# Kernel optimization log

Hardware: AMD Instinct MI355X
Metric: run time of the kernel (lower is better)

## Reference

```python
import jax, jax.numpy as jnp
import numpy as np

L, B, T, D, H = 12, 8, 512, 768, 12
DH = D // H
EPS = 1e-12


def _layernorm(x, w, b):
    u = jnp.mean(x, axis=-1, keepdims=True)
    s = jnp.mean(jnp.square(x - u), axis=-1, keepdims=True)
    return w * ((x - u) / jnp.sqrt(s + EPS)) + b


def setup_inputs() -> dict:
    key = jax.random.key(0)
    ks = jax.random.split(key, 8)
    w = lambda k: jax.random.normal(k, (L, D, D), dtype=jnp.float32) * 0.02
    return {
        "query_states": jax.random.normal(ks[0], (B, T, D), dtype=jnp.float32),
        "hidden_states": jax.random.normal(ks[1], (B, T, D), dtype=jnp.float32),
        "attention_mask": jnp.zeros((B, 1, 1, T), dtype=jnp.float32),
        "Wq": w(ks[2]), "bq": jnp.zeros((L, D), jnp.float32),
        "Wk": w(ks[3]), "bk": jnp.zeros((L, D), jnp.float32),
        "Wv": w(ks[4]), "bv": jnp.zeros((L, D), jnp.float32),
        "Wo1": w(ks[5]), "bo1": jnp.zeros((L, D), jnp.float32),
        "ln1_w": jnp.ones((L, D), jnp.float32), "ln1_b": jnp.zeros((L, D), jnp.float32),
        "Wo2": w(ks[6]), "bo2": jnp.zeros((L, D), jnp.float32),
        "ln2_w": jnp.ones((L, D), jnp.float32), "ln2_b": jnp.zeros((L, D), jnp.float32),
    }


def reference(query_states, hidden_states, attention_mask,
              Wq, bq, Wk, bk, Wv, bv,
              Wo1, bo1, ln1_w, ln1_b,
              Wo2, bo2, ln2_w, ln2_b):
    scale = 1.0 / jnp.sqrt(jnp.float32(DH))

    def heads(x):  # [B,T,D] -> [B,H,T,DH]
        return x.reshape(B, T, H, DH).transpose(0, 2, 1, 3)

    def layer_fn(hidden, p):
        (wq, bq_, wk, bk_, wv, bv_, wo1, bo1_, l1w, l1b, wo2, bo2_, l2w, l2b) = p
        q = heads(query_states @ wq + bq_)
        k = heads(hidden @ wk + bk_)
        v = heads(hidden @ wv + bv_)
        scores = jnp.einsum("bhqd,bhkd->bhqk", q, k) * scale + attention_mask
        probs = jax.nn.softmax(scores, axis=-1)
        ctx = jnp.einsum("bhqk,bhkd->bhqd", probs, v)
        ctx = ctx.transpose(0, 2, 1, 3).reshape(B, T, D)
        # attention Output: LN(dense(ctx) + key_states)
        attn_out = _layernorm(ctx @ wo1 + bo1_ + hidden, l1w, l1b)
        # layer Output (intermediate is identity in source): LN(dense(attn_out) + attn_out)
        out = _layernorm(attn_out @ wo2 + bo2_ + attn_out, l2w, l2b)
        return out, None

    params = (Wq, bq, Wk, bk, Wv, bv, Wo1, bo1, ln1_w, ln1_b, Wo2, bo2, ln2_w, ln2_b)
    hidden, _ = jax.lax.scan(layer_fn, hidden_states, params)
    return hidden
```

## Files before the change

### kernel.cpp

```cpp
#include <hip/hip_runtime.h>
#include <stdint.h>

#define L_ 12
#define B_ 8
#define T_ 512
#define D_ 768
#define H_ 12
#define DH_ 64
#define M_ 4096
#define DD_ (D_*D_)

typedef unsigned short u16;
typedef __bf16 bf16x8 __attribute__((ext_vector_type(8)));
typedef float f32x4 __attribute__((ext_vector_type(4)));
typedef u16 u16x4 __attribute__((ext_vector_type(4)));
typedef u16 u16x8 __attribute__((ext_vector_type(8)));

static __device__ __forceinline__ u16 f2b(float f) {
  union { float f; unsigned u; } x; x.f = f;
  unsigned r = x.u + 0x7fffu + ((x.u >> 16) & 1u);
  return (u16)(r >> 16);
}
static __device__ __forceinline__ float b2f(u16 u) {
  union { unsigned u; float f; } x; x.u = ((unsigned)u) << 16; return x.f;
}
static __device__ __forceinline__ void gload16(u16* lds, const u16* g) {
  __builtin_amdgcn_global_load_lds((__attribute__((address_space(1))) void*)(g),
                                   (__attribute__((address_space(3))) void*)(lds), 16, 0, 0);
}
static __device__ __forceinline__ f32x4 mfma16(bf16x8 a, bf16x8 b, f32x4 c) {
  return __builtin_amdgcn_mfma_f32_16x16x32_bf16(a, b, c, 0, 0, 0);
}
static __device__ __forceinline__ bf16x8 ldfrag(const u16* p) {
  return *reinterpret_cast<const bf16x8*>(p);
}

__global__ void init_kernel(const float* __restrict__ qs, const float* __restrict__ hs,
                            u16* __restrict__ qsb, u16* __restrict__ hidb, int n) {
  int i = blockIdx.x * 256 + threadIdx.x;
  if (i < n) {
    qsb[i] = f2b(qs[i]);
    hidb[i] = f2b(hs[i]);
  }
}

__global__ void wt_kernel(const float* W0, const float* W1, const float* W2,
                          const float* W3, const float* W4, u16* __restrict__ out) {
  const int z = blockIdx.z, layer = z / 5, w = z % 5;
  const float* base = (w == 0) ? W0 : (w == 1) ? W1 : (w == 2) ? W2 : (w == 3) ? W3 : W4;
  const float* W = base + (size_t)layer * DD_;
  u16* O = out + (size_t)z * DD_;
  const int nb = blockIdx.x * 64, kb = blockIdx.y * 64;
  __shared__ u16 tile[64][66];
  const int tid = threadIdx.x;
  #pragma unroll
  for (int p = 0; p < 4; ++p) {
    const int idx = p * 256 + tid;
    const int kr = idx >> 4, n4 = (idx & 15) * 4;
    const f32x4 v4 = *reinterpret_cast<const f32x4*>(W + (size_t)(kb + kr) * D_ + nb + n4);
    #pragma unroll
    for (int i = 0; i < 4; i++) tile[n4 + i][kr] = f2b(v4[i]);
  }
  __syncthreads();
  #pragma unroll
  for (int p = 0; p < 4; ++p) {
    const int idx = p * 256 + tid;
    const int n = idx >> 4, k4 = (idx & 15) * 4;
    u16x4 o4;
    #pragma unroll
    for (int i = 0; i < 4; i++) o4[i] = tile[n][k4 + i];
    *reinterpret_cast<u16x4*>(O + (size_t)(nb + n) * D_ + kb + k4) = o4;
  }
}

static __device__ void gemm_core(const u16* __restrict__ A, const u16* __restrict__ W,
                                 const float* __restrict__ bias, const u16* __restrict__ resb,
                                 float* __restrict__ outf, u16* __restrict__ outb,
                                 u16* __restrict__ outv) {
  __shared__ __align__(16) u16 lA[2][64 * 64];
  __shared__ __align__(16) u16 lB[2][128 * 64];
  const int tid = threadIdx.x;
  const int wave = tid >> 6, lane = tid & 63;
  const int wm = wave >> 1, wn = wave & 1;

  const int nbx = gridDim.x;
  const int nwg = nbx * gridDim.y;
  const int orig = blockIdx.y * nbx + blockIdx.x;
  const int cpx = nwg >> 3;
  const int swz = (orig & 7) * cpx + (orig >> 3);
  const int m0 = (swz / nbx) * 64, n0 = (swz % nbx) * 128;
  const int lr = lane & 15, lg = lane >> 4;

  f32x4 acc[2][4];
  #pragma unroll
  for (int i = 0; i < 2; i++)
    #pragma unroll
    for (int j = 0; j < 4; j++) acc[i][j] = f32x4{0.f, 0.f, 0.f, 0.f};

  const int uA0 = wave * 64 + lane, uA1 = 256 + uA0;
  const int rA0 = uA0 >> 3, cA0 = ((uA0 & 7) ^ (rA0 & 7)) << 3;
  const int rA1 = uA1 >> 3, cA1 = ((uA1 & 7) ^ (rA1 & 7)) << 3;
  const u16* Ab0 = A + (size_t)(m0 + rA0) * D_ + cA0;
  const u16* Ab1 = A + (size_t)(m0 + rA1) * D_ + cA1;
  const u16* Wb[4];
  #pragma unroll
  for (int q = 0; q < 4; ++q) {
    const int u = q * 256 + wave * 64 + lane;
    const int r = u >> 3, c = ((u & 7) ^ (r & 7)) << 3;
    Wb[q] = W + (size_t)(n0 + r) * D_ + c;
  }

#define STAGE(buf, k0_) do {                                   \
    gload16(lA[buf] + wave * 512,        Ab0 + (k0_));         \
    gload16(lA[buf] + 2048 + wave * 512, Ab1 + (k0_));         \
    gload16(lB[buf] + wave * 512,        Wb[0] + (k0_));       \
    gload16(lB[buf] + 2048 + wave * 512, Wb[1] + (k0_));       \
    gload16(lB[buf] + 4096 + wave * 512, Wb[2] + (k0_));       \
    gload16(lB[buf] + 6144 + wave * 512, Wb[3] + (k0_));       \
  } while (0)

  STAGE(0, 0);
  __syncthreads();

  const int sx = lr & 7;

  int cur = 0;
  for (int kt = 0; kt < 12; ++kt) {
    if (kt < 11) STAGE(cur ^ 1, (kt + 1) * 64);
    bf16x8 af[2][2], bw[2][4];
    #pragma unroll
    for (int kk = 0; kk < 2; ++kk) {
      const int uo = ((kk * 4 + lg) ^ sx) << 3;
      #pragma unroll
      for (int i = 0; i < 2; i++)
        af[kk][i] = ldfrag(lA[cur] + ((wm * 32 + i * 16 + lr) << 6) + uo);
      #pragma unroll
      for (int j = 0; j < 4; j++)
        bw[kk][j] = ldfrag(lB[cur] + ((wn * 64 + j * 16 + lr) << 6) + uo);
    }
    #pragma unroll
    for (int kk = 0; kk < 2; ++kk)
      #pragma unroll
      for (int i = 0; i < 2; i++)
        #pragma unroll
        for (int j = 0; j < 4; j++)
          acc[i][j] = mfma16(af[kk][i], bw[kk][j], acc[i][j]);
    __syncthreads();
    cur ^= 1;
  }
#undef STAGE

  if (outv) {
    #pragma unroll
    for (int j = 0; j < 4; j++) {
      const int colg = n0 + wn * 64 + j * 16 + lr;
      const float bv = bias[colg];
      const int h = colg >> 6, dh = colg & 63;
      #pragma unroll
      for (int i = 0; i < 2; i++) {
        const int rowb = m0 + wm * 32 + i * 16 + lg * 4;
        const int bb = rowb >> 9, t = rowb & 511;
        u16x4 o4;
        #pragma unroll
        for (int r = 0; r < 4; r++) o4[r] = f2b(acc[i][j][r] + bv);
        *reinterpret_cast<u16x4*>(outv + ((size_t)((bb * H_ + h) * DH_ + dh)) * T_ + t) = o4;
      }
    }
    return;
  }
  #pragma unroll
  for (int j = 0; j < 4; j++) {
    const int colg = n0 + wn * 64 + j * 16 + lr;
    const float bv = bias[colg];
    #pragma unroll
    for (int i = 0; i < 2; i++) {
      const int rowb = m0 + wm * 32 + i * 16 + lg * 4;
      #pragma unroll
      for (int r = 0; r < 4; r++) {
        float v = acc[i][j][r] + bv;
        const size_t off = (size_t)(rowb + r) * D_ + colg;
        if (resb) v += b2f(resb[off]);
        if (outf) outf[off] = v;
        if (outb) outb[off] = f2b(v);
      }
    }
  }
}

__global__ __launch_bounds__(256) void qall_kernel(const u16* qsb, const u16* wt60,
                                                   const float* bq, u16* qall) {
  const int l = blockIdx.z;
  gemm_core(qsb, wt60 + (size_t)l * 5 * DD_, bq + l * D_, nullptr,
            nullptr, qall + (size_t)l * M_ * D_, nullptr);
}

__global__ __launch_bounds__(256) void kv_kernel(const u16* hidb,
                                                 const u16* wk, const u16* wv,
                                                 const float* bk, const float* bv,
                                                 u16* kout, u16* vtout) {
  if (blockIdx.z == 0) gemm_core(hidb, wk, bk, nullptr, nullptr, kout, nullptr);
  else                 gemm_core(hidb, wv, bv, nullptr, nullptr, nullptr, vtout);
}

__global__ __launch_bounds__(256) void qkv3_kernel(const u16* qsb, const u16* hidb,
                                                   const u16* wq, const u16* wk, const u16* wv,
                                                   const float* bq, const float* bk, const float* bv,
                                                   u16* q, u16* kout, u16* vtout) {
  if (blockIdx.z == 0)      gemm_core(qsb,  wq, bq, nullptr, nullptr, q, nullptr);
  else if (blockIdx.z == 1) gemm_core(hidb, wk, bk, nullptr, nullptr, kout, nullptr);
  else                      gemm_core(hidb, wv, bv, nullptr, nullptr, nullptr, vtout);
}

__global__ __launch_bounds__(256) void o_kernel(const u16* A, const u16* W, const float* bias,
                                                const u16* resb, float* outf) {
  gemm_core(A, W, bias, resb, outf, nullptr, nullptr);
}

__global__ __launch_bounds__(256) void attn_kernel(const u16* __restrict__ q, const u16* __restrict__ k,
                                                   const u16* __restrict__ vt, const float* __restrict__ mask,
                                                   u16* __restrict__ ctx) {
  __shared__ __align__(16) u16 KT[2][64 * 64];
  __shared__ __align__(16) u16 VT[2][64 * 64];
  __shared__ __align__(16) u16 PT[4 * 16 * 64];
  const int tid = threadIdx.x, wave = tid >> 6, lane = tid & 63;
  const int id = blockIdx.x;
  const int bh = id % 96, qblk = id / 96;
  const int b = bh / H_, h = bh % H_;
  const int q0 = qblk * 64 + wave * 16;
  const int lr = lane & 15, lg = lane >> 4;

  bf16x8 qa0, qa1;
  {
    const u16* qp = q + (size_t)(b * T_ + q0 + lr) * D_ + h * DH_ + lg * 8;
    qa0 = ldfrag(qp);
    qa1 = ldfrag(qp + 32);
  }

  const int su0 = wave * 64 + lane, su1 = 256 + wave * 64 + lane;
  const int sr0 = su0 >> 3, sc0 = ((su0 & 7) ^ (sr0 & 7)) << 3;
  const int sr1 = su1 >> 3, sc1 = ((su1 & 7) ^ (sr1 & 7)) << 3;
  const u16* kbase = k + (size_t)b * T_ * D_ + h * DH_;
  const u16* vbase = vt + (size_t)bh * DH_ * T_;

#define STAGEKV(buf, kt_) do {                                                         \
    gload16(KT[buf] + wave * 512,        kbase + (size_t)((kt_) * 64 + sr0) * D_ + sc0); \
    gload16(KT[buf] + 2048 + wave * 512, kbase + (size_t)((kt_) * 64 + sr1) * D_ + sc1); \
    gload16(VT[buf] + wave * 512,        vbase + (size_t)sr0 * T_ + (kt_) * 64 + sc0);   \
    gload16(VT[buf] + 2048 + wave * 512, vbase + (size_t)sr1 * T_ + (kt_) * 64 + sc1);   \
  } while (0)

  float mrow[4] = {-1e30f, -1e30f, -1e30f, -1e30f};
  float lrow[4] = {0.f, 0.f, 0.f, 0.f};
  f32x4 O[4] = { {0,0,0,0}, {0,0,0,0}, {0,0,0,0}, {0,0,0,0} };
  u16* Pw = PT + wave * 1024;

  STAGEKV(0, 0);
  int cur = 0;
  for (int kt = 0; kt < 8; ++kt) {
    __syncthreads();
    if (kt < 7) STAGEKV(cur ^ 1, kt + 1);

    f32x4 S[4];
    #pragma unroll
    for (int nf = 0; nf < 4; ++nf) {
      const u16* kr = KT[cur] + (nf * 16 + lr) * 64;
      bf16x8 kb0 = ldfrag(kr + ((lg       ^ (lr & 7)) << 3));
      bf16x8 kb1 = ldfrag(kr + (((4 + lg) ^ (lr & 7)) << 3));
      f32x4 a = {0.f, 0.f, 0.f, 0.f};
      a = mfma16(qa0, kb0, a);
      a = mfma16(qa1, kb1, a);
      S[nf] = a;
    }
    #pragma unroll
    for (int nf = 0; nf < 4; ++nf) {
      const float mk = mask[(size_t)b * T_ + kt * 64 + nf * 16 + lr];
      #pragma unroll
      for (int r = 0; r < 4; r++) S[nf][r] = S[nf][r] * 0.125f + mk;
    }
    #pragma unroll
    for (int r = 0; r < 4; r++) {
      float tm = fmaxf(fmaxf(S[0][r], S[1][r]), fmaxf(S[2][r], S[3][r]));
      #pragma unroll
      for (int d = 1; d <= 8; d <<= 1) tm = fmaxf(tm, __shfl_xor(tm, d));
      const float mn = fmaxf(mrow[r], tm);
      const float sc = __expf(mrow[r] - mn);
      float ts = 0.f;
      #pragma unroll
      for (int nf = 0; nf < 4; ++nf) { float pv = __expf(S[nf][r] - mn); S[nf][r] = pv; ts += pv; }
      #pragma unroll
      for (int d = 1; d <= 8; d <<= 1) ts += __shfl_xor(ts, d);
      lrow[r] = lrow[r] * sc + ts;
      mrow[r] = mn;
      #pragma unroll
      for (int nf = 0; nf < 4; ++nf) O[nf][r] *= sc;
    }
    #pragma unroll
    for (int nf = 0; nf < 4; ++nf)
      #pragma unroll
      for (int r = 0; r < 4; r++) {
        const int R = lg * 4 + r;
        Pw[R * 64 + ((((nf << 1) | (lr >> 3)) ^ (R & 7)) << 3) + (lr & 7)] = f2b(S[nf][r]);
      }
    #pragma unroll
    for (int ks = 0; ks < 2; ++ks) {
      bf16x8 pa = ldfrag(Pw + lr * 64 + (((ks * 4 + lg) ^ (lr & 7)) << 3));
      #pragma unroll
      for (int nf = 0; nf < 4; ++nf) {
        bf16x8 vb = ldfrag(VT[cur] + (nf * 16 + lr) * 64 + (((ks * 4 + lg) ^ (lr & 7)) << 3));
        O[nf] = mfma16(pa, vb, O[nf]);
      }
    }
    cur ^= 1;
  }
#undef STAGEKV

  #pragma unroll
  for (int r = 0; r < 4; r++) {
    const float inv = 1.f / lrow[r];
    const int row = q0 + lg * 4 + r;
    #pragma unroll
    for (int nf = 0; nf < 4; ++nf)
      ctx[(size_t)(b * T_ + row) * D_ + h * DH_ + nf * 16 + lr] = f2b(O[nf][r] * inv);
  }
}

__global__ __launch_bounds__(256) void ln_kernel(const float* __restrict__ y,
                                                 const float* __restrict__ w, const float* __restrict__ bp,
                                                 float* __restrict__ outf, u16* __restrict__ outb) {
  const int wave = threadIdx.x >> 6, lane = threadIdx.x & 63;
  const int row = blockIdx.x * 4 + wave;
  const f32x4* yp = (const f32x4*)(y + (size_t)row * D_);
  f32x4 x[3];
  #pragma unroll
  for (int j = 0; j < 3; j++) x[j] = yp[j * 64 + lane];
  float s = 0.f;
  #pragma unroll
  for (int j = 0; j < 3; j++) s += x[j][0] + x[j][1] + x[j][2] + x[j][3];
  #pragma unroll
  for (int d = 1; d <= 32; d <<= 1) s += __shfl_xor(s, d);
  const float u = s * (1.f / D_);
  float v = 0.f;
  #pragma unroll
  for (int j = 0; j < 3; j++)
    #pragma unroll
    for (int c = 0; c < 4; c++) { float t = x[j][c] - u; v += t * t; }
  #pragma unroll
  for (int d = 1; d <= 32; d <<= 1) v += __shfl_xor(v, d);
  const float rinv = rsqrtf(v * (1.f / D_) + 1e-12f);
  const f32x4* wp = (const f32x4*)w;
  const f32x4* bpp = (const f32x4*)bp;
  #pragma unroll
  for (int j = 0; j < 3; j++) {
    const f32x4 w4 = wp[j * 64 + lane];
    const f32x4 b4 = bpp[j * 64 + lane];
    f32x4 o4;
    u16x4 ob;
    #pragma unroll
    for (int c = 0; c < 4; c++) {
      o4[c] = w4[c] * ((x[j][c] - u) * rinv) + b4[c];
      ob[c] = f2b(o4[c]);
    }
    if (outf) ((f32x4*)(outf + (size_t)row * D_))[j * 64 + lane] = o4;
    ((u16x4*)(outb + (size_t)row * D_))[j * 64 + lane] = ob;
  }
}

extern "C" void kernel_launch(void* const* d_in, const int* in_sizes, int n_in,
                              void* d_out, int out_size, void* d_ws, size_t ws_size,
                              hipStream_t stream) {
  const float* qs   = (const float*)d_in[0];
  const float* hs   = (const float*)d_in[1];
  const float* mask = (const float*)d_in[2];
  const float* Wq   = (const float*)d_in[3];
  const float* bq   = (const float*)d_in[4];
  const float* Wk   = (const float*)d_in[5];
  const float* bk   = (const float*)d_in[6];
  const float* Wv   = (const float*)d_in[7];
  const float* bv   = (const float*)d_in[8];
  const float* Wo1  = (const float*)d_in[9];
  const float* bo1  = (const float*)d_in[10];
  const float* l1w  = (const float*)d_in[11];
  const float* l1b  = (const float*)d_in[12];
  const float* Wo2  = (const float*)d_in[13];
  const float* bo2  = (const float*)d_in[14];
  const float* l2w  = (const float*)d_in[15];
  const float* l2b  = (const float*)d_in[16];
  float* out = (float*)d_out;

  char* p = (char*)d_ws;
  auto alloc = [&](size_t bytes) { char* r = p; p += (bytes + 255) & ~(size_t)255; return r; };
  u16*   qsb  = (u16*)alloc((size_t)M_ * D_ * 2);
  u16*   hidb = (u16*)alloc((size_t)M_ * D_ * 2);
  u16*   kb_  = (u16*)alloc((size_t)M_ * D_ * 2);
  u16*   vtb  = (u16*)alloc((size_t)M_ * D_ * 2);
  u16*   ctxb = (u16*)alloc((size_t)M_ * D_ * 2);
  float* y    = (float*)alloc((size_t)M_ * D_ * 4);
  u16*   aob  = (u16*)alloc((size_t)M_ * D_ * 2);
  u16*   qb   = (u16*)alloc((size_t)M_ * D_ * 2);
  const size_t base_used = (size_t)(p - (char*)d_ws);
  const size_t wt60_bytes = (size_t)60 * DD_ * 2;
  const size_t qall_bytes = (size_t)12 * M_ * D_ * 2;
  const bool wt_once  = (ws_size - base_used) >= wt60_bytes + 512;
  u16* wt60 = (u16*)alloc(wt_once ? wt60_bytes : (size_t)5 * DD_ * 2);
  const size_t used2 = (size_t)(p - (char*)d_ws);
  const bool q_all   = wt_once && (ws_size - used2) >= qall_bytes + 512;
  u16* qall = q_all ? (u16*)alloc(qall_bytes) : qb;

  init_kernel<<<(M_ * D_ + 255) / 256, 256, 0, stream>>>(qs, hs, qsb, hidb, M_ * D_);
  if (wt_once)
    wt_kernel<<<dim3(12, 12, 60), 256, 0, stream>>>(Wq, Wk, Wv, Wo1, Wo2, wt60);
  if (q_all)
    qall_kernel<<<dim3(6, 64, 12), 256, 0, stream>>>(qsb, wt60, bq, qall);

  for (int l = 0; l < L_; ++l) {
    const size_t wo = (size_t)l * DD_;
    u16* wt = wt_once ? (wt60 + (size_t)l * 5 * DD_) : wt60;
    if (!wt_once)
      wt_kernel<<<dim3(12, 12, 5), 256, 0, stream>>>(Wq + wo, Wk + wo, Wv + wo, Wo1 + wo, Wo2 + wo, wt);
    const u16* qcur;
    if (q_all) {
      qcur = qall + (size_t)l * M_ * D_;
      kv_kernel<<<dim3(6, 64, 2), 256, 0, stream>>>(hidb, wt + DD_, wt + 2 * DD_,
                                                    bk + l * D_, bv + l * D_, kb_, vtb);
    } else {
      qcur = qb;
      qkv3_kernel<<<dim3(6, 64, 3), 256, 0, stream>>>(qsb, hidb,
          wt, wt + DD_, wt + 2 * DD_, bq + l * D_, bk + l * D_, bv + l * D_, qb, kb_, vtb);
    }
    attn_kernel<<<768, 256, 0, stream>>>(qcur, kb_, vtb, mask, ctxb);
    o_kernel<<<dim3(6, 64), 256, 0, stream>>>(ctxb, wt + 3 * DD_, bo1 + l * D_, hidb, y);
    ln_kernel<<<1024, 256, 0, stream>>>(y, l1w + l * D_, l1b + l * D_, nullptr, aob);
    o_kernel<<<dim3(6, 64), 256, 0, stream>>>(aob, wt + 4 * DD_, bo2 + l * D_, aob, y);
    ln_kernel<<<1024, 256, 0, stream>>>(y, l2w + l * D_, l2b + l * D_,
                                        (l == L_ - 1) ? out : nullptr, hidb);
  }
}
```

Measured before the change: 1.326 ms.

## Add 128x128 GEMM for hoisted Q projection, bf16 pre-LN buffer, attention setprio

Adds a 128x128-tile GEMM core with workgroup swizzling and uses it for the hoisted all-layer Q projection, halving that grid. Stores the pre-layernorm sums in bf16 rather than fp32, which halves the y traffic but adds rounding before LayerNorm. Raises wave priority around the MFMA blocks in attention and pairs rows in the weight transpose so LDS stores are 32-bit. These are several loosely related tweaks, and the bf16 intermediate reduces accuracy.

Result: faster. 1.115 ms, median of 2 (-15.9%).

```diff
diff --git a/kernel.cpp b/kernel.cpp
--- a/kernel.cpp
+++ b/kernel.cpp
@@ -13,8 +13,8 @@
 typedef unsigned short u16;
 typedef __bf16 bf16x8 __attribute__((ext_vector_type(8)));
 typedef float f32x4 __attribute__((ext_vector_type(4)));
+typedef u16 u16x2 __attribute__((ext_vector_type(2)));
 typedef u16 u16x4 __attribute__((ext_vector_type(4)));
-typedef u16 u16x8 __attribute__((ext_vector_type(8)));
 
 static __device__ __forceinline__ u16 f2b(float f) {
   union { float f; unsigned u; } x; x.f = f;
@@ -54,12 +54,16 @@
   __shared__ u16 tile[64][66];
   const int tid = threadIdx.x;
   #pragma unroll
-  for (int p = 0; p < 4; ++p) {
+  for (int p = 0; p < 2; ++p) {
     const int idx = p * 256 + tid;
-    const int kr = idx >> 4, n4 = (idx & 15) * 4;
-    const f32x4 v4 = *reinterpret_cast<const f32x4*>(W + (size_t)(kb + kr) * D_ + nb + n4);
-    #pragma unroll
-    for (int i = 0; i < 4; i++) tile[n4 + i][kr] = f2b(v4[i]);
+    const int rp = idx >> 4, n4 = (idx & 15) * 4;
+    const f32x4 a = *reinterpret_cast<const f32x4*>(W + (size_t)(kb + 2 * rp) * D_ + nb + n4);
+    const f32x4 b = *reinterpret_cast<const f32x4*>(W + (size_t)(kb + 2 * rp + 1) * D_ + nb + n4);
+    #pragma unroll
+    for (int i = 0; i < 4; i++) {
+      u16x2 pr; pr[0] = f2b(a[i]); pr[1] = f2b(b[i]);
+      *reinterpret_cast<u16x2*>(&tile[n4 + i][2 * rp]) = pr;
+    }
   }
   __syncthreads();
   #pragma unroll
@@ -187,11 +191,96 @@
   }
 }
 
+static __device__ void gemm128_core(const u16* __restrict__ A, const u16* __restrict__ W,
+                                    const float* __restrict__ bias, u16* __restrict__ outb) {
+  __shared__ __align__(16) u16 lA[2][128 * 64];
+  __shared__ __align__(16) u16 lB[2][128 * 64];
+  const int tid = threadIdx.x;
+  const int wave = tid >> 6, lane = tid & 63;
+  const int wm = wave >> 1, wn = wave & 1;
+
+  const int nbx = gridDim.x;
+  const int nwg = nbx * gridDim.y;
+  const int orig = blockIdx.y * nbx + blockIdx.x;
+  const int cpx = nwg >> 3;
+  const int swz = (orig & 7) * cpx + (orig >> 3);
+  const int m0 = (swz / nbx) * 128, n0 = (swz % nbx) * 128;
+  const int lr = lane & 15, lg = lane >> 4;
+
+  f32x4 acc[4][4];
+  #pragma unroll
+  for (int i = 0; i < 4; i++)
+    #pragma unroll
+    for (int j = 0; j < 4; j++) acc[i][j] = f32x4{0.f, 0.f, 0.f, 0.f};
+
+  const u16* Ab[4];
+  const u16* Wb[4];
+  #pragma unroll
+  for (int q = 0; q < 4; ++q) {
+    const int u = q * 256 + wave * 64 + lane;
+    const int r = u >> 3, c = ((u & 7) ^ (r & 7)) << 3;
+    Ab[q] = A + (size_t)(m0 + r) * D_ + c;
+    Wb[q] = W + (size_t)(n0 + r) * D_ + c;
+  }
+
+#define STAGE128(buf, k0_) do {                                \
+    gload16(lA[buf] + wave * 512,        Ab[0] + (k0_));       \
+    gload16(lA[buf] + 2048 + wave * 512, Ab[1] + (k0_));       \
+    gload16(lA[buf] + 4096 + wave * 512, Ab[2] + (k0_));       \
+    gload16(lA[buf] + 6144 + wave * 512, Ab[3] + (k0_));       \
+    gload16(lB[buf] + wave * 512,        Wb[0] + (k0_));       \
+    gload16(lB[buf] + 2048 + wave * 512, Wb[1] + (k0_));       \
+    gload16(lB[buf] + 4096 + wave * 512, Wb[2] + (k0_));       \
+    gload16(lB[buf] + 6144 + wave * 512, Wb[3] + (k0_));       \
+  } while (0)
+
+  STAGE128(0, 0);
+  __syncthreads();
+
+  const int sx = lr & 7;
+
+  int cur = 0;
+  for (int kt = 0; kt < 12; ++kt) {
+    if (kt < 11) STAGE128(cur ^ 1, (kt + 1) * 64);
+    #pragma unroll
+    for (int kk = 0; kk < 2; ++kk) {
+      const int uo = ((kk * 4 + lg) ^ sx) << 3;
+      bf16x8 af[4], bw[4];
+      #pragma unroll
+      for (int i = 0; i < 4; i++)
+        af[i] = ldfrag(lA[cur] + ((wm * 64 + i * 16 + lr) << 6) + uo);
+      #pragma unroll
+      for (int j = 0; j < 4; j++)
+        bw[j] = ldfrag(lB[cur] + ((wn * 64 + j * 16 + lr) << 6) + uo);
+      #pragma unroll
+      for (int i = 0; i < 4; i++)
+        #pragma unroll
+        for (int j = 0; j < 4; j++)
+          acc[i][j] = mfma16(af[i], bw[j], acc[i][j]);
+    }
+    __syncthreads();
+    cur ^= 1;
+  }
+#undef STAGE128
+
+  #pragma unroll
+  for (int j = 0; j < 4; j++) {
+    const int colg = n0 + wn * 64 + j * 16 + lr;
+    const float bv = bias[colg];
+    #pragma unroll
+    for (int i = 0; i < 4; i++) {
+      const int rowb = m0 + wm * 64 + i * 16 + lg * 4;
+      #pragma unroll
+      for (int r = 0; r < 4; r++)
+        outb[(size_t)(rowb + r) * D_ + colg] = f2b(acc[i][j][r] + bv);
+    }
+  }
+}
+
 __global__ __launch_bounds__(256) void qall_kernel(const u16* qsb, const u16* wt60,
                                                    const float* bq, u16* qall) {
   const int l = blockIdx.z;
-  gemm_core(qsb, wt60 + (size_t)l * 5 * DD_, bq + l * D_, nullptr,
-            nullptr, qall + (size_t)l * M_ * D_, nullptr);
+  gemm128_core(qsb, wt60 + (size_t)l * 5 * DD_, bq + l * D_, qall + (size_t)l * M_ * D_);
 }
 
 __global__ __launch_bounds__(256) void kv_kernel(const u16* hidb,
@@ -212,8 +301,8 @@
 }
 
 __global__ __launch_bounds__(256) void o_kernel(const u16* A, const u16* W, const float* bias,
-                                                const u16* resb, float* outf) {
-  gemm_core(A, W, bias, resb, outf, nullptr, nullptr);
+                                                const u16* resb, u16* yb) {
+  gemm_core(A, W, bias, resb, nullptr, yb, nullptr);
 }
 
 __global__ __launch_bounds__(256) void attn_kernel(const u16* __restrict__ q, const u16* __restrict__ k,
@@ -261,6 +350,7 @@
     if (kt < 7) STAGEKV(cur ^ 1, kt + 1);
 
     f32x4 S[4];
+    __builtin_amdgcn_s_setprio(1);
     #pragma unroll
     for (int nf = 0; nf < 4; ++nf) {
       const u16* kr = KT[cur] + (nf * 16 + lr) * 64;
@@ -271,6 +361,7 @@
       a = mfma16(qa1, kb1, a);
       S[nf] = a;
     }
+    __builtin_amdgcn_s_setprio(0);
     #pragma unroll
     for (int nf = 0; nf < 4; ++nf) {
       const float mk = mask[(size_t)b * T_ + kt * 64 + nf * 16 + lr];
@@ -301,6 +392,7 @@
         const int R = lg * 4 + r;
         Pw[R * 64 + ((((nf << 1) | (lr >> 3)) ^ (R & 7)) << 3) + (lr & 7)] = f2b(S[nf][r]);
       }
+    __builtin_amdgcn_s_setprio(1);
     #pragma unroll
     for (int ks = 0; ks < 2; ++ks) {
       bf16x8 pa = ldfrag(Pw + lr * 64 + (((ks * 4 + lg) ^ (lr & 7)) << 3));
@@ -310,6 +402,7 @@
         O[nf] = mfma16(pa, vb, O[nf]);
       }
     }
+    __builtin_amdgcn_s_setprio(0);
     cur ^= 1;
   }
 #undef STAGEKV
@@ -324,15 +417,19 @@
   }
 }
 
-__global__ __launch_bounds__(256) void ln_kernel(const float* __restrict__ y,
+__global__ __launch_bounds__(256) void ln_kernel(const u16* __restrict__ y,
                                                  const float* __restrict__ w, const float* __restrict__ bp,
                                                  float* __restrict__ outf, u16* __restrict__ outb) {
   const int wave = threadIdx.x >> 6, lane = threadIdx.x & 63;
   const int row = blockIdx.x * 4 + wave;
-  const f32x4* yp = (const f32x4*)(y + (size_t)row * D_);
+  const u16x4* yp = (const u16x4*)(y + (size_t)row * D_);
   f32x4 x[3];
   #pragma unroll
-  for (int j = 0; j < 3; j++) x[j] = yp[j * 64 + lane];
+  for (int j = 0; j < 3; j++) {
+    const u16x4 r4 = yp[j * 64 + lane];
+    #pragma unroll
+    for (int c = 0; c < 4; c++) x[j][c] = b2f(r4[c]);
+  }
   float s = 0.f;
   #pragma unroll
   for (int j = 0; j < 3; j++) s += x[j][0] + x[j][1] + x[j][2] + x[j][3];
@@ -394,7 +491,7 @@
   u16*   kb_  = (u16*)alloc((size_t)M_ * D_ * 2);
   u16*   vtb  = (u16*)alloc((size_t)M_ * D_ * 2);
   u16*   ctxb = (u16*)alloc((size_t)M_ * D_ * 2);
-  float* y    = (float*)alloc((size_t)M_ * D_ * 4);
+  u16*   yb   = (u16*)alloc((size_t)M_ * D_ * 2);
   u16*   aob  = (u16*)alloc((size_t)M_ * D_ * 2);
   u16*   qb   = (u16*)alloc((size_t)M_ * D_ * 2);
   const size_t base_used = (size_t)(p - (char*)d_ws);
@@ -410,7 +507,7 @@
   if (wt_once)
     wt_kernel<<<dim3(12, 12, 60), 256, 0, stream>>>(Wq, Wk, Wv, Wo1, Wo2, wt60);
   if (q_all)
-    qall_kernel<<<dim3(6, 64, 12), 256, 0, stream>>>(qsb, wt60, bq, qall);
+    qall_kernel<<<dim3(6, 32, 12), 256, 0, stream>>>(qsb, wt60, bq, qall);
 
   for (int l = 0; l < L_; ++l) {
     const size_t wo = (size_t)l * DD_;
@@ -428,10 +525,10 @@
           wt, wt + DD_, wt + 2 * DD_, bq + l * D_, bk + l * D_, bv + l * D_, qb, kb_, vtb);
     }
     attn_kernel<<<768, 256, 0, stream>>>(qcur, kb_, vtb, mask, ctxb);
-    o_kernel<<<dim3(6, 64), 256, 0, stream>>>(ctxb, wt + 3 * DD_, bo1 + l * D_, hidb, y);
-    ln_kernel<<<1024, 256, 0, stream>>>(y, l1w + l * D_, l1b + l * D_, nullptr, aob);
-    o_kernel<<<dim3(6, 64), 256, 0, stream>>>(aob, wt + 4 * DD_, bo2 + l * D_, aob, y);
-    ln_kernel<<<1024, 256, 0, stream>>>(y, l2w + l * D_, l2b + l * D_,
+    o_kernel<<<dim3(6, 64), 256, 0, stream>>>(ctxb, wt + 3 * DD_, bo1 + l * D_, hidb, yb);
+    ln_kernel<<<1024, 256, 0, stream>>>(yb, l1w + l * D_, l1b + l * D_, nullptr, aob);
+    o_kernel<<<dim3(6, 64), 256, 0, stream>>>(aob, wt + 4 * DD_, bo2 + l * D_, aob, yb);
+    ln_kernel<<<1024, 256, 0, stream>>>(yb, l2w + l * D_, l2b + l * D_,
                                         (l == L_ - 1) ? out : nullptr, hidb);
   }
 }
```
